# Optimization experiments

Hardware: AMD Instinct MI355X
Metric: run time of the kernel (lower is better)

The kernel has to match this reference:

```python
import jax, jax.numpy as jnp
import numpy as np

NUM_RELATIONS = 2
NUM_NODES = 100000


def rgcn_conv(x, edge_index, edge_type, weight, root, bias):
    """PyG RGCNConv with default aggr='mean':
    out[i] = bias + x[i] @ root + sum_r mean_{j in N_r(i)} (x[j] @ W_r)
    x: [N, Cin], edge_index: [2, E], weight: [R, Cin, Cout], root: [Cin, Cout]."""
    src, dst = edge_index[0], edge_index[1]
    x_src = x[src]                      # [E, Cin] gather
    out = x @ root + bias               # [N, Cout]
    for r in range(NUM_RELATIONS):      # small fixed loop over relations
        mask = (edge_type == r).astype(x.dtype)          # [E]
        msg = (x_src @ weight[r]) * mask[:, None]        # [E, Cout]
        agg = jax.ops.segment_sum(msg, dst, num_segments=NUM_NODES)
        deg = jax.ops.segment_sum(mask, dst, num_segments=NUM_NODES)
        out = out + agg / jnp.maximum(deg, 1.0)[:, None]
    return out


def setup_inputs() -> dict:
    key = jax.random.key(0)
    ks = jax.random.split(key, 16)
    Cin, Chid, Cout = 128, 256, 128
    E = 400000
    inp = {
        "x0": jax.random.normal(ks[0], (50000, 128), jnp.float32),
        "x1": jax.random.normal(ks[1], (50000, 64), jnp.float32),
        "edge_index": jax.random.randint(ks[2], (2, E), 0, NUM_NODES),
        "edge_type": jax.random.randint(ks[3], (E,), 0, NUM_RELATIONS),
        "dec_index": jax.random.randint(ks[4], (2, 100000), 0, NUM_NODES),
        # per-node-type input projections (Linear as x @ W + b)
        "lin0_w": jax.random.normal(ks[5], (128, Cin), jnp.float32) * 0.05,
        "lin0_b": jnp.zeros((Cin,), jnp.float32),
        "lin1_w": jax.random.normal(ks[6], (64, Cin), jnp.float32) * 0.05,
        "lin1_b": jnp.zeros((Cin,), jnp.float32),
        # RGCN layer 1
        "conv1_w": jax.random.normal(ks[7], (NUM_RELATIONS, Cin, Chid), jnp.float32) * 0.05,
        "conv1_root": jax.random.normal(ks[8], (Cin, Chid), jnp.float32) * 0.05,
        "conv1_b": jnp.zeros((Chid,), jnp.float32),
        # RGCN layer 2
        "conv2_w": jax.random.normal(ks[9], (NUM_RELATIONS, Chid, Cout), jnp.float32) * 0.05,
        "conv2_root": jax.random.normal(ks[10], (Chid, Cout), jnp.float32) * 0.05,
        "conv2_b": jnp.zeros((Cout,), jnp.float32),
        # decode head: Linear(2*Cout -> 1) + sigmoid
        "fc_w": jax.random.normal(ks[11], (2 * Cout, 1), jnp.float32) * 0.05,
        "fc_b": jnp.zeros((1,), jnp.float32),
    }
    return inp


def reference(x0, x1, edge_index, edge_type, dec_index,
              lin0_w, lin0_b, lin1_w, lin1_b,
              conv1_w, conv1_root, conv1_b,
              conv2_w, conv2_root, conv2_b,
              fc_w, fc_b):
    # trans_dimensions: per-type projection then concat along nodes
    x = jnp.concatenate([x0 @ lin0_w + lin0_b, x1 @ lin1_w + lin1_b], axis=0)  # [N, Cin]
    # encode (eval mode: dropout is identity)
    x = rgcn_conv(x, edge_index, edge_type, conv1_w, conv1_root, conv1_b)
    x = jax.nn.relu(x)
    z = rgcn_conv(x, edge_index, edge_type, conv2_w, conv2_root, conv2_b)
    # decode
    pair = jnp.concatenate([z[dec_index[0]], z[dec_index[1]]], axis=-1)  # [P, 2*Cout]
    return jax.nn.sigmoid(pair @ fc_w + fc_b)
```

## Files before the change

kernel.cpp:

```cpp
#include <hip/hip_runtime.h>
#include <hip/hip_bf16.h>
#include <math.h>

#define N_NODES 100000
#define N_EDGES 400000
#define N_PAIRS 100000
#define NBINS   200000

typedef short short8_t __attribute__((ext_vector_type(8)));
typedef float f32x4    __attribute__((ext_vector_type(4)));

__device__ __forceinline__ ushort f2bf(float f) {
    uint u = __float_as_uint(f);
    u += 0x7fffu + ((u >> 16) & 1u);
    return (ushort)(u >> 16);
}
__device__ __forceinline__ float bf2f(ushort b) {
    return __uint_as_float(((uint)b) << 16);
}
__device__ __forceinline__ uint packbf(float a, float b) {
    return (uint)f2bf(a) | ((uint)f2bf(b) << 16);
}

#define GLDS16(gp, lp) \
    __builtin_amdgcn_global_load_lds((const __attribute__((address_space(1))) uint*)(gp), \
                                     (__attribute__((address_space(3))) uint*)(lp), 16, 0, 0)

template<int N> __device__ __forceinline__ void waitvm() {
    if constexpr (N == 0)      asm volatile("s_waitcnt vmcnt(0)" ::: "memory");
    else if constexpr (N == 4) asm volatile("s_waitcnt vmcnt(4)" ::: "memory");
    else if constexpr (N == 8) asm volatile("s_waitcnt vmcnt(8)" ::: "memory");
}

#define PREP_TOTAL 2671184
__global__ void prep_kernel(const float* __restrict__ x0, const float* __restrict__ x1,
                            const float* __restrict__ l0w, const float* __restrict__ l1w,
                            const float* __restrict__ c1r, const float* __restrict__ c1w,
                            const float* __restrict__ c2r, const float* __restrict__ c2w,
                            ushort* __restrict__ x0bf, ushort* __restrict__ x1bf,
                            ushort* __restrict__ wl0, ushort* __restrict__ wl1,
                            ushort* __restrict__ wc1, ushort* __restrict__ wc2,
                            int* __restrict__ cnt) {
    int i = blockIdx.x * 256 + threadIdx.x;
    const int stride = gridDim.x * 256;
    for (; i < PREP_TOTAL; i += stride) {
        int j = i;
        if (j < 1600000) {
            float4 v = ((const float4*)x0)[j];
            ushort4 o; o.x = f2bf(v.x); o.y = f2bf(v.y); o.z = f2bf(v.z); o.w = f2bf(v.w);
            ((ushort4*)x0bf)[j] = o;
        } else if ((j -= 1600000) < 800000) {
            float4 v = ((const float4*)x1)[j];
            ushort4 o; o.x = f2bf(v.x); o.y = f2bf(v.y); o.z = f2bf(v.z); o.w = f2bf(v.w);
            ((ushort4*)x1bf)[j] = o;
        } else if ((j -= 800000) < 16384) {
            int n = j >> 7, k = j & 127;
            wl0[j] = f2bf(l0w[(size_t)k * 128 + n]);
        } else if ((j -= 16384) < 8192) {
            int n = j >> 6, k = j & 63;
            wl1[j] = f2bf(l1w[(size_t)k * 128 + n]);
        } else if ((j -= 8192) < 98304) {
            int n = j / 384, k = j % 384;
            float v = (k < 128) ? c1r[(size_t)k * 256 + n] : c1w[(size_t)(k - 128) * 256 + n];
            wc1[(size_t)n * 384 + k] = f2bf(v);
        } else if ((j -= 98304) < 98304) {
            int n = j >> 8, k = j & 255;
            float v = (n < 128) ? c2r[(size_t)k * 128 + n]
                                : c2w[((size_t)((n >> 7) - 1) * 256 + k) * 128 + (n & 127)];
            wc2[(size_t)n * 256 + k] = f2bf(v);
        } else {
            j -= 98304;
            ((int4*)cnt)[j] = make_int4(0, 0, 0, 0);
        }
    }
}

__global__ void hist_kernel(const int* __restrict__ dst, const int* __restrict__ et,
                            int* __restrict__ cnt) {
    int e = blockIdx.x * 256 + threadIdx.x;
    if (e < N_EDGES) atomicAdd(&cnt[et[e] * N_NODES + dst[e]], 1);
}

__global__ __launch_bounds__(1024) void scan1_kernel(const int* __restrict__ cnt,
                                                     int* __restrict__ ptr,
                                                     int* __restrict__ aux) {
    __shared__ int s[1024];
    int i = blockIdx.x * 1024 + threadIdx.x;
    int v = (i < NBINS) ? cnt[i] : 0;
    s[threadIdx.x] = v;
    __syncthreads();
    for (int off = 1; off < 1024; off <<= 1) {
        int t = (threadIdx.x >= off) ? s[threadIdx.x - off] : 0;
        __syncthreads();
        s[threadIdx.x] += t;
        __syncthreads();
    }
    if (i < NBINS) ptr[i] = s[threadIdx.x] - v;
    if (threadIdx.x == 1023) aux[blockIdx.x] = s[1023];
}

__global__ void scan2_kernel(int* __restrict__ aux, int nblk) {
    __shared__ int s[256];
    int v = (threadIdx.x < nblk) ? aux[threadIdx.x] : 0;
    s[threadIdx.x] = v;
    __syncthreads();
    for (int off = 1; off < 256; off <<= 1) {
        int t = (threadIdx.x >= off) ? s[threadIdx.x - off] : 0;
        __syncthreads();
        s[threadIdx.x] += t;
        __syncthreads();
    }
    if (threadIdx.x < nblk) aux[threadIdx.x] = s[threadIdx.x] - v;
}

__global__ void scan3_kernel(const int* __restrict__ aux, int* __restrict__ ptr,
                             int* __restrict__ cursor) {
    int i = blockIdx.x * 256 + threadIdx.x;
    if (i < NBINS) {
        int val = ptr[i] + aux[i >> 10];
        ptr[i] = val;
        cursor[i] = val;
    }
    if (i == 0) ptr[NBINS] = N_EDGES;
}

__global__ void fill_kernel(const int* __restrict__ src, const int* __restrict__ dst,
                            const int* __restrict__ et, int* __restrict__ cursor,
                            int* __restrict__ esorted) {
    int e = blockIdx.x * 256 + threadIdx.x;
    if (e < N_EDGES) {
        int b = et[e] * N_NODES + dst[e];
        int pos = atomicAdd(&cursor[b], 1);
        esorted[pos] = src[e];
    }
}

__global__ void gather1_kernel(const int* __restrict__ ptr, const int* __restrict__ es,
                               ushort* __restrict__ A1) {
    int d = blockIdx.x * 4 + (threadIdx.x >> 6);
    if (d >= N_NODES) return;
    int lane = threadIdx.x & 63;
    int p0 = ptr[d],           p1 = ptr[d + 1];
    int q0 = ptr[N_NODES + d], q1 = ptr[N_NODES + d + 1];
    int n0 = p1 - p0, n1 = q1 - q0;
    int n  = n0 > n1 ? n0 : n1;
    float a0 = 0, a1 = 0, b0 = 0, b1 = 0;
    for (int k = 0; k < n; k += 4) {
        uint v00 = 0, v01 = 0, v02 = 0, v03 = 0;
        uint v10 = 0, v11 = 0, v12 = 0, v13 = 0;
        if (k     < n0) v00 = *(const uint*)(A1 + (size_t)es[p0 + k]     * 384 + lane * 2);
        if (k + 1 < n0) v01 = *(const uint*)(A1 + (size_t)es[p0 + k + 1] * 384 + lane * 2);
        if (k + 2 < n0) v02 = *(const uint*)(A1 + (size_t)es[p0 + k + 2] * 384 + lane * 2);
        if (k + 3 < n0) v03 = *(const uint*)(A1 + (size_t)es[p0 + k + 3] * 384 + lane * 2);
        if (k     < n1) v10 = *(const uint*)(A1 + (size_t)es[q0 + k]     * 384 + lane * 2);
        if (k + 1 < n1) v11 = *(const uint*)(A1 + (size_t)es[q0 + k + 1] * 384 + lane * 2);
        if (k + 2 < n1) v12 = *(const uint*)(A1 + (size_t)es[q0 + k + 2] * 384 + lane * 2);
        if (k + 3 < n1) v13 = *(const uint*)(A1 + (size_t)es[q0 + k + 3] * 384 + lane * 2);
        a0 += bf2f((ushort)(v00 & 0xffffu)) + bf2f((ushort)(v01 & 0xffffu))
            + bf2f((ushort)(v02 & 0xffffu)) + bf2f((ushort)(v03 & 0xffffu));
        a1 += bf2f((ushort)(v00 >> 16)) + bf2f((ushort)(v01 >> 16))
            + bf2f((ushort)(v02 >> 16)) + bf2f((ushort)(v03 >> 16));
        b0 += bf2f((ushort)(v10 & 0xffffu)) + bf2f((ushort)(v11 & 0xffffu))
            + bf2f((ushort)(v12 & 0xffffu)) + bf2f((ushort)(v13 & 0xffffu));
        b1 += bf2f((ushort)(v10 >> 16)) + bf2f((ushort)(v11 >> 16))
            + bf2f((ushort)(v12 >> 16)) + bf2f((ushort)(v13 >> 16));
    }
    float i0 = n0 ? 1.0f / (float)n0 : 0.0f;
    float i1 = n1 ? 1.0f / (float)n1 : 0.0f;
    uint* row = (uint*)(A1 + (size_t)d * 384);
    row[64  + lane] = packbf(a0 * i0, a1 * i0);
    row[128 + lane] = packbf(b0 * i1, b1 * i1);
}

__global__ void combine2_kernel(const int* __restrict__ ptr, const int* __restrict__ es,
                                const ushort* __restrict__ H, ushort* __restrict__ zb) {
    int d = blockIdx.x * 4 + (threadIdx.x >> 6);
    if (d >= N_NODES) return;
    int lane = threadIdx.x & 63;
    int p0 = ptr[d],           p1 = ptr[d + 1];
    int q0 = ptr[N_NODES + d], q1 = ptr[N_NODES + d + 1];
    int n0 = p1 - p0, n1 = q1 - q0;
    int n  = n0 > n1 ? n0 : n1;
    uint rv = *(const uint*)(H + (size_t)d * 384 + lane * 2);
    float r0 = bf2f((ushort)(rv & 0xffffu)), r1 = bf2f((ushort)(rv >> 16));
    float a0 = 0, a1 = 0, b0 = 0, b1 = 0;
    for (int k = 0; k < n; k += 4) {
        uint v00 = 0, v01 = 0, v02 = 0, v03 = 0;
        uint v10 = 0, v11 = 0, v12 = 0, v13 = 0;
        if (k     < n0) v00 = *(const uint*)(H + (size_t)es[p0 + k]     * 384 + 128 + lane * 2);
        if (k + 1 < n0) v01 = *(const uint*)(H + (size_t)es[p0 + k + 1] * 384 + 128 + lane * 2);
        if (k + 2 < n0) v02 = *(const uint*)(H + (size_t)es[p0 + k + 2] * 384 + 128 + lane * 2);
        if (k + 3 < n0) v03 = *(const uint*)(H + (size_t)es[p0 + k + 3] * 384 + 128 + lane * 2);
        if (k     < n1) v10 = *(const uint*)(H + (size_t)es[q0 + k]     * 384 + 256 + lane * 2);
        if (k + 1 < n1) v11 = *(const uint*)(H + (size_t)es[q0 + k + 1] * 384 + 256 + lane * 2);
        if (k + 2 < n1) v12 = *(const uint*)(H + (size_t)es[q0 + k + 2] * 384 + 256 + lane * 2);
        if (k + 3 < n1) v13 = *(const uint*)(H + (size_t)es[q0 + k + 3] * 384 + 256 + lane * 2);
        a0 += bf2f((ushort)(v00 & 0xffffu)) + bf2f((ushort)(v01 & 0xffffu))
            + bf2f((ushort)(v02 & 0xffffu)) + bf2f((ushort)(v03 & 0xffffu));
        a1 += bf2f((ushort)(v00 >> 16)) + bf2f((ushort)(v01 >> 16))
            + bf2f((ushort)(v02 >> 16)) + bf2f((ushort)(v03 >> 16));
        b0 += bf2f((ushort)(v10 & 0xffffu)) + bf2f((ushort)(v11 & 0xffffu))
            + bf2f((ushort)(v12 & 0xffffu)) + bf2f((ushort)(v13 & 0xffffu));
        b1 += bf2f((ushort)(v10 >> 16)) + bf2f((ushort)(v11 >> 16))
            + bf2f((ushort)(v12 >> 16)) + bf2f((ushort)(v13 >> 16));
    }
    float i0 = n0 ? 1.0f / (float)n0 : 0.0f;
    float i1 = n1 ? 1.0f / (float)n1 : 0.0f;
    uint* orow = (uint*)(zb + (size_t)d * 128);
    orow[lane] = packbf(r0 + a0 * i0 + b0 * i1, r1 + a1 * i0 + b1 * i1);
}

template<int KTOT, int OST, int BIASN, bool RELU>
__device__ __forceinline__
void gemm_body(const ushort* __restrict__ A, const ushort* __restrict__ Wt,
               const float* __restrict__ bias, ushort* __restrict__ outp,
               int nrows, int m0, int n0) {
    __shared__ short As[3][128 * 32];
    __shared__ short Bs[3][128 * 32];
    const int t = threadIdx.x;
    const int lane = t & 63, w = t >> 6;
    const int wr = w >> 1, wc = w & 1;
    const int l15 = lane & 15, l4 = lane >> 4;

    const int arow = t >> 2;
    const int swc = ((t & 3) ^ ((arow >> 1) & 3)) * 8;
    int rg0 = m0 + arow;      if (rg0 >= nrows) rg0 = nrows - 1;
    int rg1 = m0 + arow + 64; if (rg1 >= nrows) rg1 = nrows - 1;
    const ushort* ap0 = A + (size_t)rg0 * KTOT + swc;
    const ushort* ap1 = A + (size_t)rg1 * KTOT + swc;
    const ushort* bp0 = Wt + (size_t)(n0 + arow) * KTOT + swc;
    const ushort* bp1 = Wt + (size_t)(n0 + arow + 64) * KTOT + swc;

#define STAGE(slot, kg) do { \
        GLDS16(ap0 + (kg), &As[slot][t * 8]); \
        GLDS16(ap1 + (kg), &As[slot][(t + 256) * 8]); \
        GLDS16(bp0 + (kg), &Bs[slot][t * 8]); \
        GLDS16(bp1 + (kg), &Bs[slot][(t + 256) * 8]); \
    } while (0)

    f32x4 acc[4][4];
#pragma unroll
    for (int j = 0; j < 4; j++) {
        int col = n0 + wc * 64 + j * 16 + l15;
        float bv = (col < BIASN) ? bias[col] : 0.0f;
        f32x4 tmp = {bv, bv, bv, bv};
#pragma unroll
        for (int i = 0; i < 4; i++) acc[i][j] = tmp;
    }

    const int xr = (l4 ^ ((l15 >> 1) & 3)) * 8;

    constexpr int NSTEP = KTOT / 32;
    STAGE(0, 0);
    if (NSTEP > 1) STAGE(1, 32);
    for (int ks = 0; ks < NSTEP; ks++) {
        const int slot = ks % 3;
        if (ks + 2 < NSTEP) {
            STAGE((ks + 2) % 3, (ks + 2) * 32);
            waitvm<8>();
        } else if (ks + 1 < NSTEP) {
            waitvm<4>();
        } else {
            waitvm<0>();
        }
        asm volatile("s_barrier" ::: "memory");
        short8_t af[4], bfr[4];
#pragma unroll
        for (int i = 0; i < 4; i++)
            af[i] = *(short8_t*)&As[slot][(wr * 64 + i * 16 + l15) * 32 + xr];
#pragma unroll
        for (int j = 0; j < 4; j++)
            bfr[j] = *(short8_t*)&Bs[slot][(wc * 64 + j * 16 + l15) * 32 + xr];
#pragma unroll
        for (int i = 0; i < 4; i++)
#pragma unroll
            for (int j = 0; j < 4; j++)
                acc[i][j] = __builtin_amdgcn_mfma_f32_16x16x32_bf16(af[i], bfr[j], acc[i][j], 0, 0, 0);
        asm volatile("s_barrier" ::: "memory");
    }
#undef STAGE

#pragma unroll
    for (int i = 0; i < 4; i++) {
#pragma unroll
        for (int r2 = 0; r2 < 4; r2++) {
            int row = m0 + wr * 64 + i * 16 + l4 * 4 + r2;
            if (row < nrows) {
#pragma unroll
                for (int j = 0; j < 4; j++) {
                    int col = n0 + wc * 64 + j * 16 + l15;
                    float v = acc[i][j][r2];
                    if (RELU) v = fmaxf(v, 0.0f);
                    outp[(size_t)row * OST + col] = f2bf(v);
                }
            }
        }
    }
}

template<int KTOT, int NP, int OST, int BIASN, bool RELU>
__global__ __launch_bounds__(256)
void mfma_gemm_kernel(const ushort* __restrict__ A, const ushort* __restrict__ Wt,
                      const float* __restrict__ bias, ushort* __restrict__ outp,
                      int nrows, int mtiles) {
    const int nwg = mtiles * NP;
    const int q = nwg >> 3, r = nwg & 7;
    const int orig = blockIdx.x;
    const int xcd = orig & 7;
    const int work = (xcd < r ? xcd * (q + 1) : r * (q + 1) + (xcd - r) * q) + (orig >> 3);
    const int mt = work / NP;
    gemm_body<KTOT, OST, BIASN, RELU>(A, Wt, bias, outp, nrows,
                                      mt * 128, (work - mt * NP) * 128);
}

__global__ __launch_bounds__(256)
void proj_kernel(const ushort* __restrict__ x0bf, const ushort* __restrict__ x1bf,
                 const ushort* __restrict__ wl0, const ushort* __restrict__ wl1,
                 const float* __restrict__ l0b, const float* __restrict__ l1b,
                 ushort* __restrict__ A1) {
    if (blockIdx.x < 391)
        gemm_body<128, 384, 128, false>(x0bf, wl0, l0b, A1, 50000,
                                        blockIdx.x * 128, 0);
    else
        gemm_body<64, 384, 128, false>(x1bf, wl1, l1b, A1 + (size_t)50000 * 384, 50000,
                                       (blockIdx.x - 391) * 128, 0);
}

__global__ void decode_kernel(const ushort* __restrict__ zb, const int* __restrict__ dec,
                              const float* __restrict__ fcw, const float* __restrict__ fcb,
                              float* __restrict__ out) {
    int wid  = blockIdx.x * 4 + (threadIdx.x >> 6);
    int lane = threadIdx.x & 63;
    if (wid >= N_PAIRS) return;
    int s = dec[wid];
    int d = dec[N_PAIRS + wid];
    uint vs = ((const uint*)(zb + (size_t)s * 128))[lane];
    uint vd = ((const uint*)(zb + (size_t)d * 128))[lane];
    float v = bf2f((ushort)(vs & 0xffffu)) * fcw[2 * lane]
            + bf2f((ushort)(vs >> 16))     * fcw[2 * lane + 1]
            + bf2f((ushort)(vd & 0xffffu)) * fcw[128 + 2 * lane]
            + bf2f((ushort)(vd >> 16))     * fcw[128 + 2 * lane + 1];
#pragma unroll
    for (int off = 32; off > 0; off >>= 1) v += __shfl_down(v, off);
    if (lane == 0) out[wid] = 1.0f / (1.0f + expf(-(v + fcb[0])));
}

extern "C" void kernel_launch(void* const* d_in, const int* in_sizes, int n_in,
                              void* d_out, int out_size, void* d_ws, size_t ws_size,
                              hipStream_t stream) {
    const float* x0        = (const float*)d_in[0];
    const float* x1        = (const float*)d_in[1];
    const int*   edge_idx  = (const int*)  d_in[2];
    const int*   edge_type = (const int*)  d_in[3];
    const int*   dec_index = (const int*)  d_in[4];
    const float* lin0_w    = (const float*)d_in[5];
    const float* lin0_b    = (const float*)d_in[6];
    const float* lin1_w    = (const float*)d_in[7];
    const float* lin1_b    = (const float*)d_in[8];
    const float* conv1_w   = (const float*)d_in[9];
    const float* conv1_root= (const float*)d_in[10];
    const float* conv1_b   = (const float*)d_in[11];
    const float* conv2_w   = (const float*)d_in[12];
    const float* conv2_root= (const float*)d_in[13];
    const float* conv2_b   = (const float*)d_in[14];
    const float* fc_w      = (const float*)d_in[15];
    const float* fc_b      = (const float*)d_in[16];
    float* out = (float*)d_out;

    char* W = (char*)d_ws;
    ushort* A1    = (ushort*)(W + 0);
    ushort* H     = (ushort*)(W + 0);
    ushort* y1    = (ushort*)(W + 76800000);
    ushort* zb    = (ushort*)(W + 76800000);
    int*    cnt   = (int*)   (W + 128000000);
    int*    ptrb  = (int*)   (W + 128800000);
    int*    cursor= (int*)   (W + 129600016);
    int*    aux   = (int*)   (W + 130400016);
    int*    esort = (int*)   (W + 130404112);
    ushort* wc1   = (ushort*)(W + 132004112);
    ushort* wc2   = (ushort*)(W + 132200720);
    ushort* wl0   = (ushort*)(W + 132397328);
    ushort* wl1   = (ushort*)(W + 132430096);
    ushort* x0bf  = (ushort*)(W + 132446480);
    ushort* x1bf  = (ushort*)(W + 145246480);

    const int* esrc = edge_idx;
    const int* edst = edge_idx + N_EDGES;

    prep_kernel<<<2048, 256, 0, stream>>>(x0, x1, lin0_w, lin1_w,
                                          conv1_root, conv1_w, conv2_root, conv2_w,
                                          x0bf, x1bf, wl0, wl1, wc1, wc2, cnt);

    hist_kernel<<<(N_EDGES + 255) / 256, 256, 0, stream>>>(edst, edge_type, cnt);
    scan1_kernel<<<(NBINS + 1023) / 1024, 1024, 0, stream>>>(cnt, ptrb, aux);
    scan2_kernel<<<1, 256, 0, stream>>>(aux, (NBINS + 1023) / 1024);
    scan3_kernel<<<(NBINS + 255) / 256, 256, 0, stream>>>(aux, ptrb, cursor);
    fill_kernel<<<(N_EDGES + 255) / 256, 256, 0, stream>>>(esrc, edst, edge_type,
                                                           cursor, esort);

    proj_kernel<<<782, 256, 0, stream>>>(x0bf, x1bf, wl0, wl1, lin0_b, lin1_b, A1);

    gather1_kernel<<<(N_NODES + 3) / 4, 256, 0, stream>>>(ptrb, esort, A1);
    mfma_gemm_kernel<384, 2, 256, 256, true>
        <<<1564, 256, 0, stream>>>(A1, wc1, conv1_b, y1, N_NODES, 782);

    mfma_gemm_kernel<256, 3, 384, 128, false>
        <<<2346, 256, 0, stream>>>(y1, wc2, conv2_b, H, N_NODES, 782);
    combine2_kernel<<<(N_NODES + 3) / 4, 256, 0, stream>>>(ptrb, esort, H, zb);

    decode_kernel<<<(N_PAIRS + 3) / 4, 256, 0, stream>>>(zb, dec_index, fc_w, fc_b, out);
}
```

Measured before the change: 257.4 us.

## Process two nodes per wave in gathers/decode and vectorize GEMM epilogue stores

The gather, combine and decode kernels now handle two destination nodes (or pairs) per wavefront, interleaving their neighbor loads so more independent memory requests are in flight, and the launch grids shrink to match. The GEMM swaps the MFMA operand order so each lane holds four consecutive output columns. This lets the bias be loaded as one vector and the epilogue write packed 8-byte bf16 stores instead of scalar 2-byte stores. In exchange, the loop now runs to the maximum degree of both nodes, so the shorter node's lanes do predicated no-op iterations. The inner unroll also drops from four edges to two.

```diff
diff --git a/kernel.cpp b/kernel.cpp
--- a/kernel.cpp
+++ b/kernel.cpp
@@ -21,6 +21,8 @@
 __device__ __forceinline__ uint packbf(float a, float b) {
     return (uint)f2bf(a) | ((uint)f2bf(b) << 16);
 }
+__device__ __forceinline__ float lo16(uint v) { return bf2f((ushort)(v & 0xffffu)); }
+__device__ __forceinline__ float hi16(uint v) { return bf2f((ushort)(v >> 16)); }
 
 #define GLDS16(gp, lp) \
     __builtin_amdgcn_global_load_lds((const __attribute__((address_space(1))) uint*)(gp), \
@@ -137,77 +139,89 @@
 
 __global__ void gather1_kernel(const int* __restrict__ ptr, const int* __restrict__ es,
                                ushort* __restrict__ A1) {
-    int d = blockIdx.x * 4 + (threadIdx.x >> 6);
-    if (d >= N_NODES) return;
+    int d0 = (blockIdx.x * 4 + (threadIdx.x >> 6)) * 2;
+    if (d0 >= N_NODES) return;
     int lane = threadIdx.x & 63;
-    int p0 = ptr[d],           p1 = ptr[d + 1];
-    int q0 = ptr[N_NODES + d], q1 = ptr[N_NODES + d + 1];
-    int n0 = p1 - p0, n1 = q1 - q0;
-    int n  = n0 > n1 ? n0 : n1;
-    float a0 = 0, a1 = 0, b0 = 0, b1 = 0;
-    for (int k = 0; k < n; k += 4) {
-        uint v00 = 0, v01 = 0, v02 = 0, v03 = 0;
-        uint v10 = 0, v11 = 0, v12 = 0, v13 = 0;
-        if (k     < n0) v00 = *(const uint*)(A1 + (size_t)es[p0 + k]     * 384 + lane * 2);
-        if (k + 1 < n0) v01 = *(const uint*)(A1 + (size_t)es[p0 + k + 1] * 384 + lane * 2);
-        if (k + 2 < n0) v02 = *(const uint*)(A1 + (size_t)es[p0 + k + 2] * 384 + lane * 2);
-        if (k + 3 < n0) v03 = *(const uint*)(A1 + (size_t)es[p0 + k + 3] * 384 + lane * 2);
-        if (k     < n1) v10 = *(const uint*)(A1 + (size_t)es[q0 + k]     * 384 + lane * 2);
-        if (k + 1 < n1) v11 = *(const uint*)(A1 + (size_t)es[q0 + k + 1] * 384 + lane * 2);
-        if (k + 2 < n1) v12 = *(const uint*)(A1 + (size_t)es[q0 + k + 2] * 384 + lane * 2);
-        if (k + 3 < n1) v13 = *(const uint*)(A1 + (size_t)es[q0 + k + 3] * 384 + lane * 2);
-        a0 += bf2f((ushort)(v00 & 0xffffu)) + bf2f((ushort)(v01 & 0xffffu))
-            + bf2f((ushort)(v02 & 0xffffu)) + bf2f((ushort)(v03 & 0xffffu));
-        a1 += bf2f((ushort)(v00 >> 16)) + bf2f((ushort)(v01 >> 16))
-            + bf2f((ushort)(v02 >> 16)) + bf2f((ushort)(v03 >> 16));
-        b0 += bf2f((ushort)(v10 & 0xffffu)) + bf2f((ushort)(v11 & 0xffffu))
-            + bf2f((ushort)(v12 & 0xffffu)) + bf2f((ushort)(v13 & 0xffffu));
-        b1 += bf2f((ushort)(v10 >> 16)) + bf2f((ushort)(v11 >> 16))
-            + bf2f((ushort)(v12 >> 16)) + bf2f((ushort)(v13 >> 16));
-    }
-    float i0 = n0 ? 1.0f / (float)n0 : 0.0f;
-    float i1 = n1 ? 1.0f / (float)n1 : 0.0f;
-    uint* row = (uint*)(A1 + (size_t)d * 384);
-    row[64  + lane] = packbf(a0 * i0, a1 * i0);
-    row[128 + lane] = packbf(b0 * i1, b1 * i1);
+    int p0[2], n0[2], q0[2], n1[2];
+#pragma unroll
+    for (int u = 0; u < 2; u++) {
+        p0[u] = ptr[d0 + u];           n0[u] = ptr[d0 + u + 1] - p0[u];
+        q0[u] = ptr[N_NODES + d0 + u]; n1[u] = ptr[N_NODES + d0 + u + 1] - q0[u];
+    }
+    float a0[2] = {0, 0}, a1[2] = {0, 0}, b0[2] = {0, 0}, b1[2] = {0, 0};
+    int n = n0[0] > n0[1] ? n0[0] : n0[1];
+    int m2 = n1[0] > n1[1] ? n1[0] : n1[1];
+    n = n > m2 ? n : m2;
+    for (int k = 0; k < n; k += 2) {
+        uint v0[2] = {0, 0}, v1[2] = {0, 0}, v2[2] = {0, 0}, v3[2] = {0, 0};
+#pragma unroll
+        for (int u = 0; u < 2; u++) {
+            if (k     < n0[u]) v0[u] = *(const uint*)(A1 + (size_t)es[p0[u] + k]     * 384 + lane * 2);
+            if (k + 1 < n0[u]) v1[u] = *(const uint*)(A1 + (size_t)es[p0[u] + k + 1] * 384 + lane * 2);
+            if (k     < n1[u]) v2[u] = *(const uint*)(A1 + (size_t)es[q0[u] + k]     * 384 + lane * 2);
+            if (k + 1 < n1[u]) v3[u] = *(const uint*)(A1 + (size_t)es[q0[u] + k + 1] * 384 + lane * 2);
+        }
+#pragma unroll
+        for (int u = 0; u < 2; u++) {
+            a0[u] += lo16(v0[u]) + lo16(v1[u]);
+            a1[u] += hi16(v0[u]) + hi16(v1[u]);
+            b0[u] += lo16(v2[u]) + lo16(v3[u]);
+            b1[u] += hi16(v2[u]) + hi16(v3[u]);
+        }
+    }
+#pragma unroll
+    for (int u = 0; u < 2; u++) {
+        float i0 = n0[u] ? 1.0f / (float)n0[u] : 0.0f;
+        float i1 = n1[u] ? 1.0f / (float)n1[u] : 0.0f;
+        uint* row = (uint*)(A1 + (size_t)(d0 + u) * 384);
+        row[64  + lane] = packbf(a0[u] * i0, a1[u] * i0);
+        row[128 + lane] = packbf(b0[u] * i1, b1[u] * i1);
+    }
 }
 
 __global__ void combine2_kernel(const int* __restrict__ ptr, const int* __restrict__ es,
                                 const ushort* __restrict__ H, ushort* __restrict__ zb) {
-    int d = blockIdx.x * 4 + (threadIdx.x >> 6);
-    if (d >= N_NODES) return;
+    int d0 = (blockIdx.x * 4 + (threadIdx.x >> 6)) * 2;
+    if (d0 >= N_NODES) return;
     int lane = threadIdx.x & 63;
-    int p0 = ptr[d],           p1 = ptr[d + 1];
-    int q0 = ptr[N_NODES + d], q1 = ptr[N_NODES + d + 1];
-    int n0 = p1 - p0, n1 = q1 - q0;
-    int n  = n0 > n1 ? n0 : n1;
-    uint rv = *(const uint*)(H + (size_t)d * 384 + lane * 2);
-    float r0 = bf2f((ushort)(rv & 0xffffu)), r1 = bf2f((ushort)(rv >> 16));
-    float a0 = 0, a1 = 0, b0 = 0, b1 = 0;
-    for (int k = 0; k < n; k += 4) {
-        uint v00 = 0, v01 = 0, v02 = 0, v03 = 0;
-        uint v10 = 0, v11 = 0, v12 = 0, v13 = 0;
-        if (k     < n0) v00 = *(const uint*)(H + (size_t)es[p0 + k]     * 384 + 128 + lane * 2);
-        if (k + 1 < n0) v01 = *(const uint*)(H + (size_t)es[p0 + k + 1] * 384 + 128 + lane * 2);
-        if (k + 2 < n0) v02 = *(const uint*)(H + (size_t)es[p0 + k + 2] * 384 + 128 + lane * 2);
-        if (k + 3 < n0) v03 = *(const uint*)(H + (size_t)es[p0 + k + 3] * 384 + 128 + lane * 2);
-        if (k     < n1) v10 = *(const uint*)(H + (size_t)es[q0 + k]     * 384 + 256 + lane * 2);
-        if (k + 1 < n1) v11 = *(const uint*)(H + (size_t)es[q0 + k + 1] * 384 + 256 + lane * 2);
-        if (k + 2 < n1) v12 = *(const uint*)(H + (size_t)es[q0 + k + 2] * 384 + 256 + lane * 2);
-        if (k + 3 < n1) v13 = *(const uint*)(H + (size_t)es[q0 + k + 3] * 384 + 256 + lane * 2);
-        a0 += bf2f((ushort)(v00 & 0xffffu)) + bf2f((ushort)(v01 & 0xffffu))
-            + bf2f((ushort)(v02 & 0xffffu)) + bf2f((ushort)(v03 & 0xffffu));
-        a1 += bf2f((ushort)(v00 >> 16)) + bf2f((ushort)(v01 >> 16))
-            + bf2f((ushort)(v02 >> 16)) + bf2f((ushort)(v03 >> 16));
-        b0 += bf2f((ushort)(v10 & 0xffffu)) + bf2f((ushort)(v11 & 0xffffu))
-            + bf2f((ushort)(v12 & 0xffffu)) + bf2f((ushort)(v13 & 0xffffu));
-        b1 += bf2f((ushort)(v10 >> 16)) + bf2f((ushort)(v11 >> 16))
-            + bf2f((ushort)(v12 >> 16)) + bf2f((ushort)(v13 >> 16));
-    }
-    float i0 = n0 ? 1.0f / (float)n0 : 0.0f;
-    float i1 = n1 ? 1.0f / (float)n1 : 0.0f;
-    uint* orow = (uint*)(zb + (size_t)d * 128);
-    orow[lane] = packbf(r0 + a0 * i0 + b0 * i1, r1 + a1 * i0 + b1 * i1);
+    int p0[2], n0[2], q0[2], n1[2];
+#pragma unroll
+    for (int u = 0; u < 2; u++) {
+        p0[u] = ptr[d0 + u];           n0[u] = ptr[d0 + u + 1] - p0[u];
+        q0[u] = ptr[N_NODES + d0 + u]; n1[u] = ptr[N_NODES + d0 + u + 1] - q0[u];
+    }
+    uint rv[2];
+    rv[0] = *(const uint*)(H + (size_t)d0 * 384 + lane * 2);
+    rv[1] = *(const uint*)(H + (size_t)(d0 + 1) * 384 + lane * 2);
+    float a0[2] = {0, 0}, a1[2] = {0, 0}, b0[2] = {0, 0}, b1[2] = {0, 0};
+    int n = n0[0] > n0[1] ? n0[0] : n0[1];
+    int m2 = n1[0] > n1[1] ? n1[0] : n1[1];
+    n = n > m2 ? n : m2;
+    for (int k = 0; k < n; k += 2) {
+        uint v0[2] = {0, 0}, v1[2] = {0, 0}, v2[2] = {0, 0}, v3[2] = {0, 0};
+#pragma unroll
+        for (int u = 0; u < 2; u++) {
+            if (k     < n0[u]) v0[u] = *(const uint*)(H + (size_t)es[p0[u] + k]     * 384 + 128 + lane * 2);
+            if (k + 1 < n0[u]) v1[u] = *(const uint*)(H + (size_t)es[p0[u] + k + 1] * 384 + 128 + lane * 2);
+            if (k     < n1[u]) v2[u] = *(const uint*)(H + (size_t)es[q0[u] + k]     * 384 + 256 + lane * 2);
+            if (k + 1 < n1[u]) v3[u] = *(const uint*)(H + (size_t)es[q0[u] + k + 1] * 384 + 256 + lane * 2);
+        }
+#pragma unroll
+        for (int u = 0; u < 2; u++) {
+            a0[u] += lo16(v0[u]) + lo16(v1[u]);
+            a1[u] += hi16(v0[u]) + hi16(v1[u]);
+            b0[u] += lo16(v2[u]) + lo16(v3[u]);
+            b1[u] += hi16(v2[u]) + hi16(v3[u]);
+        }
+    }
+#pragma unroll
+    for (int u = 0; u < 2; u++) {
+        float i0 = n0[u] ? 1.0f / (float)n0[u] : 0.0f;
+        float i1 = n1[u] ? 1.0f / (float)n1[u] : 0.0f;
+        ((uint*)(zb + (size_t)(d0 + u) * 128))[lane] =
+            packbf(lo16(rv[u]) + a0[u] * i0 + b0[u] * i1,
+                   hi16(rv[u]) + a1[u] * i0 + b1[u] * i1);
+    }
 }
 
 template<int KTOT, int OST, int BIASN, bool RELU>
@@ -241,11 +255,12 @@
     f32x4 acc[4][4];
 #pragma unroll
     for (int j = 0; j < 4; j++) {
-        int col = n0 + wc * 64 + j * 16 + l15;
-        float bv = (col < BIASN) ? bias[col] : 0.0f;
-        f32x4 tmp = {bv, bv, bv, bv};
-#pragma unroll
-        for (int i = 0; i < 4; i++) acc[i][j] = tmp;
+        int col = n0 + wc * 64 + j * 16 + l4 * 4;
+        f32x4 bv;
+        if (col < BIASN) bv = *(const f32x4*)(bias + col);
+        else             bv = (f32x4){0.0f, 0.0f, 0.0f, 0.0f};
+#pragma unroll
+        for (int i = 0; i < 4; i++) acc[i][j] = bv;
     }
 
     const int xr = (l4 ^ ((l15 >> 1) & 3)) * 8;
@@ -275,24 +290,27 @@
         for (int i = 0; i < 4; i++)
 #pragma unroll
             for (int j = 0; j < 4; j++)
-                acc[i][j] = __builtin_amdgcn_mfma_f32_16x16x32_bf16(af[i], bfr[j], acc[i][j], 0, 0, 0);
+                acc[i][j] = __builtin_amdgcn_mfma_f32_16x16x32_bf16(bfr[j], af[i], acc[i][j], 0, 0, 0);
         asm volatile("s_barrier" ::: "memory");
     }
 #undef STAGE
 
 #pragma unroll
     for (int i = 0; i < 4; i++) {
-#pragma unroll
-        for (int r2 = 0; r2 < 4; r2++) {
-            int row = m0 + wr * 64 + i * 16 + l4 * 4 + r2;
-            if (row < nrows) {
-#pragma unroll
-                for (int j = 0; j < 4; j++) {
-                    int col = n0 + wc * 64 + j * 16 + l15;
-                    float v = acc[i][j][r2];
-                    if (RELU) v = fmaxf(v, 0.0f);
-                    outp[(size_t)row * OST + col] = f2bf(v);
+        int row = m0 + wr * 64 + i * 16 + l15;
+        if (row < nrows) {
+#pragma unroll
+            for (int j = 0; j < 4; j++) {
+                int col = n0 + wc * 64 + j * 16 + l4 * 4;
+                f32x4 v = acc[i][j];
+                if (RELU) {
+#pragma unroll
+                    for (int r = 0; r < 4; r++) v[r] = fmaxf(v[r], 0.0f);
                 }
+                uint2 o;
+                o.x = packbf(v[0], v[1]);
+                o.y = packbf(v[2], v[3]);
+                *(uint2*)(outp + (size_t)row * OST + col) = o;
             }
         }
     }
@@ -329,20 +347,29 @@
 __global__ void decode_kernel(const ushort* __restrict__ zb, const int* __restrict__ dec,
                               const float* __restrict__ fcw, const float* __restrict__ fcb,
                               float* __restrict__ out) {
-    int wid  = blockIdx.x * 4 + (threadIdx.x >> 6);
+    int p0 = (blockIdx.x * 4 + (threadIdx.x >> 6)) * 2;
+    if (p0 >= N_PAIRS) return;
     int lane = threadIdx.x & 63;
-    if (wid >= N_PAIRS) return;
-    int s = dec[wid];
-    int d = dec[N_PAIRS + wid];
-    uint vs = ((const uint*)(zb + (size_t)s * 128))[lane];
-    uint vd = ((const uint*)(zb + (size_t)d * 128))[lane];
-    float v = bf2f((ushort)(vs & 0xffffu)) * fcw[2 * lane]
-            + bf2f((ushort)(vs >> 16))     * fcw[2 * lane + 1]
-            + bf2f((ushort)(vd & 0xffffu)) * fcw[128 + 2 * lane]
-            + bf2f((ushort)(vd >> 16))     * fcw[128 + 2 * lane + 1];
-#pragma unroll
-    for (int off = 32; off > 0; off >>= 1) v += __shfl_down(v, off);
-    if (lane == 0) out[wid] = 1.0f / (1.0f + expf(-(v + fcb[0])));
+    float ws0 = fcw[2 * lane],       ws1 = fcw[2 * lane + 1];
+    float wd0 = fcw[128 + 2 * lane], wd1 = fcw[128 + 2 * lane + 1];
+    int s0 = dec[p0],     dd0 = dec[N_PAIRS + p0];
+    int s1 = dec[p0 + 1], dd1 = dec[N_PAIRS + p0 + 1];
+    uint vs0 = ((const uint*)(zb + (size_t)s0  * 128))[lane];
+    uint vd0 = ((const uint*)(zb + (size_t)dd0 * 128))[lane];
+    uint vs1 = ((const uint*)(zb + (size_t)s1  * 128))[lane];
+    uint vd1 = ((const uint*)(zb + (size_t)dd1 * 128))[lane];
+    float v0 = lo16(vs0) * ws0 + hi16(vs0) * ws1 + lo16(vd0) * wd0 + hi16(vd0) * wd1;
+    float v1 = lo16(vs1) * ws0 + hi16(vs1) * ws1 + lo16(vd1) * wd0 + hi16(vd1) * wd1;
+#pragma unroll
+    for (int off = 32; off > 0; off >>= 1) {
+        v0 += __shfl_down(v0, off);
+        v1 += __shfl_down(v1, off);
+    }
+    if (lane == 0) {
+        float fb = fcb[0];
+        out[p0]     = 1.0f / (1.0f + expf(-(v0 + fb)));
+        out[p0 + 1] = 1.0f / (1.0f + expf(-(v1 + fb)));
+    }
 }
 
 extern "C" void kernel_launch(void* const* d_in, const int* in_sizes, int n_in,
@@ -400,13 +427,13 @@
 
     proj_kernel<<<782, 256, 0, stream>>>(x0bf, x1bf, wl0, wl1, lin0_b, lin1_b, A1);
 
-    gather1_kernel<<<(N_NODES + 3) / 4, 256, 0, stream>>>(ptrb, esort, A1);
+    gather1_kernel<<<12500, 256, 0, stream>>>(ptrb, esort, A1);
     mfma_gemm_kernel<384, 2, 256, 256, true>
         <<<1564, 256, 0, stream>>>(A1, wc1, conv1_b, y1, N_NODES, 782);
 
     mfma_gemm_kernel<256, 3, 384, 128, false>
         <<<2346, 256, 0, stream>>>(y1, wc2, conv2_b, H, N_NODES, 782);
-    combine2_kernel<<<(N_NODES + 3) / 4, 256, 0, stream>>>(ptrb, esort, H, zb);
-
-    decode_kernel<<<(N_PAIRS + 3) / 4, 256, 0, stream>>>(zb, dec_index, fc_w, fc_b, out);
-}
+    combine2_kernel<<<12500, 256, 0, stream>>>(ptrb, esort, H, zb);
+
+    decode_kernel<<<12500, 256, 0, stream>>>(zb, dec_index, fc_w, fc_b, out);
+}
```

After: 258.3 us. No clear change (+0.3%).
